# Performance work log

Hardware: AMD Instinct MI355X
Metric: run time of the kernel (lower is better)

The kernel has to match this reference:

```python
import jax, jax.numpy as jnp
import numpy as np

N_USERS = 50000
N_ITEMS = 50000
EMB_DIM = 64
N_EDGES = 1000000
N_LAYERS = 2
BATCH_SIZE = 50000
DECAY = 1e-4
NEG_SLOPE = 0.2


def setup_inputs() -> dict:
    key = jax.random.key(0)
    k1, k2, k3, k4, k5, k6 = jax.random.split(key, 6)
    return {
        "user_emb": jax.random.normal(k1, (N_USERS, EMB_DIM), dtype=jnp.float32) * 0.1,
        "item_emb": jax.random.normal(k2, (N_ITEMS, EMB_DIM), dtype=jnp.float32) * 0.1,
        "u_idx": jax.random.randint(k3, (N_EDGES,), 0, N_USERS),
        "i_idx": jax.random.randint(k4, (N_EDGES,), 0, N_ITEMS),
        "pos_items_ur": jax.random.randint(k5, (N_USERS,), 0, N_ITEMS),
        "neg_items_ur": jax.random.randint(k6, (N_USERS,), 0, N_ITEMS),
    }


def _segment_attn_sum(src_emb_g, e, dst, num_segments):
    # GAT-style: a = softmax_over_dst_mailbox(leaky_relu(e)); out = sum a * src_emb
    a = jax.nn.leaky_relu(e, NEG_SLOPE)
    m = jax.ops.segment_max(a, dst, num_segments=num_segments)
    m = jnp.where(jnp.isfinite(m), m, 0.0)  # empty segments -> -inf; never gathered but keep clean
    ex = jnp.exp(a - m[dst])
    den = jax.ops.segment_sum(ex, dst, num_segments=num_segments)
    w = ex / den[dst]  # den > 0 wherever an edge exists
    return jax.ops.segment_sum(w[:, None] * src_emb_g, dst, num_segments=num_segments)


def _gat_layer(user_emb, item_emb, u_idx, i_idx):
    # edge score e = <src_emb, dst_emb>, symmetric for both directions
    ue = user_emb[u_idx]           # [E, D]
    ie = item_emb[i_idx]           # [E, D]
    e = jnp.sum(ue * ie, axis=-1)  # [E]
    new_user = _segment_attn_sum(ie, e, u_idx, user_emb.shape[0])  # item -> user
    new_item = _segment_attn_sum(ue, e, i_idx, item_emb.shape[0])  # user -> item
    return new_user, new_item


def _inference(user_emb, item_emb, u_idx, i_idx):
    users = [user_emb]
    items = [item_emb]
    u, it = user_emb, item_emb
    for _ in range(N_LAYERS):
        u, it = _gat_layer(u, it, u_idx, i_idx)
        users.append(u)
        items.append(it)
    user_out = jnp.mean(jnp.stack(users, axis=1), axis=1)
    item_out = jnp.mean(jnp.stack(items, axis=1), axis=1)
    return user_out, item_out


def reference(user_emb, item_emb, u_idx, i_idx, pos_items_ur, neg_items_ur):
    user_out, item_out = _inference(user_emb, item_emb, u_idx, i_idx)
    users = user_out
    pos = item_out[pos_items_ur]
    neg = item_out[neg_items_ur]
    pos_scores = jnp.sum(users * pos, axis=1)
    neg_scores = jnp.sum(users * neg, axis=1)
    regularizer = 0.5 * (jnp.sum(users ** 2) + jnp.sum(pos ** 2) + jnp.sum(neg ** 2))
    regularizer = regularizer / BATCH_SIZE
    mf_loss = jnp.mean(jax.nn.softplus(neg_scores - pos_scores))
    emb_loss = DECAY * regularizer
    return jnp.stack([mf_loss, emb_loss])
```

## Files before the change

kernel.cpp:

```cpp
#include <hip/hip_runtime.h>
#include <math.h>

#define D 64
#define NEG_SLOPE 0.2f
#define DECAY_C 1e-4f
#define BKT_CAP 8192
#define K1_CHUNK 4096

__device__ __forceinline__ unsigned short f2bf(float f) {
  unsigned int u = __float_as_uint(f);
  u += 0x7FFFu + ((u >> 16) & 1u);
  return (unsigned short)(u >> 16);
}
__device__ __forceinline__ float bflo(unsigned int u) {
  return __uint_as_float(u << 16);
}
__device__ __forceinline__ float bfhi(unsigned int u) {
  return __uint_as_float(u & 0xFFFF0000u);
}

__global__ __launch_bounds__(256) void partition_kernel(
    const int* __restrict__ uidx, const int* __restrict__ iidx, int E,
    int nbktU, int nbktI, int* __restrict__ gCurU, int* __restrict__ gCurI,
    unsigned int* __restrict__ recU, unsigned int* __restrict__ recI,
    int npart, const float4* __restrict__ uemb,
    const float4* __restrict__ iemb, unsigned short* __restrict__ ubf,
    unsigned short* __restrict__ ibf, int nu4, int ni4) {
  if ((int)blockIdx.x >= npart) {
    int stride = ((int)gridDim.x - npart) * 256;
    int total = nu4 + ni4;
    for (int k = ((int)blockIdx.x - npart) * 256 + (int)threadIdx.x; k < total;
         k += stride) {
      bool isu = k < nu4;
      int idx = isu ? k : k - nu4;
      float4 v = isu ? uemb[idx] : iemb[idx];
      ushort4 o;
      o.x = f2bf(v.x);
      o.y = f2bf(v.y);
      o.z = f2bf(v.z);
      o.w = f2bf(v.w);
      *(ushort4*)((isu ? ubf : ibf) + (size_t)idx * 4) = o;
    }
    return;
  }
  __shared__ int uu[K1_CHUNK], ii[K1_CHUNK];
  __shared__ int histU[256], histI[256], baseU[256], baseI[256];
  int e0 = blockIdx.x * K1_CHUNK;
  int cnt = min(K1_CHUNK, E - e0);
  int t = threadIdx.x;
  for (int k = t; k < cnt; k += 256) {
    uu[k] = uidx[e0 + k];
    ii[k] = iidx[e0 + k];
  }
  histU[t] = 0;
  histI[t] = 0;
  __syncthreads();
  for (int k = t; k < cnt; k += 256) {
    atomicAdd(&histU[uu[k] >> 8], 1);
    atomicAdd(&histI[ii[k] >> 8], 1);
  }
  __syncthreads();
  {
    int h = histU[t];
    baseU[t] = (t < nbktU && h) ? atomicAdd(&gCurU[t], h) : 0;
    h = histI[t];
    baseI[t] = (t < nbktI && h) ? atomicAdd(&gCurI[t], h) : 0;
  }
  __syncthreads();
  histU[t] = 0;
  histI[t] = 0;
  __syncthreads();
  for (int k = t; k < cnt; k += 256) {
    int u = uu[k], it = ii[k];
    int b = u >> 8;
    int ofs = baseU[b] + atomicAdd(&histU[b], 1);
    if (ofs < BKT_CAP)
      recU[(size_t)b * BKT_CAP + ofs] =
          ((unsigned int)(u & 255) << 16) | (unsigned int)it;
    b = it >> 8;
    ofs = baseI[b] + atomicAdd(&histI[b], 1);
    if (ofs < BKT_CAP)
      recI[(size_t)b * BKT_CAP + ofs] =
          ((unsigned int)(it & 255) << 16) | (unsigned int)u;
  }
}

__global__ __launch_bounds__(256) void csr_kernel(
    const int* __restrict__ gCurU, const int* __restrict__ gCurI,
    const unsigned int* __restrict__ recU, const unsigned int* __restrict__ recI,
    unsigned short* __restrict__ srcU, unsigned short* __restrict__ srcI,
    int2* __restrict__ rowU, int2* __restrict__ rowI, int nbktU, int nbktI,
    int NUc, int NIc) {
  int bid = blockIdx.x;
  bool isU = bid < nbktU;
  int bkt = isU ? bid : bid - nbktU;
  const unsigned int* rec = (isU ? recU : recI) + (size_t)bkt * BKT_CAP;
  unsigned short* gsrc = (isU ? srcU : srcI) + (size_t)bkt * BKT_CAP;
  int2* rowspan = isU ? rowU : rowI;
  int N = isU ? NUc : NIc;
  int cnt = min((isU ? gCurU : gCurI)[bkt], BKT_CAP);

  __shared__ unsigned int lrec[BKT_CAP];
  __shared__ unsigned short sbuf[BKT_CAP];
  __shared__ int hist[256], excl[256], wsum[4];
  int t = threadIdx.x;
  hist[t] = 0;
  for (int k = t; k < cnt; k += 256) lrec[k] = rec[k];
  __syncthreads();
  for (int k = t; k < cnt; k += 256) atomicAdd(&hist[lrec[k] >> 16], 1);
  __syncthreads();
  int v = hist[t];
  int lane = t & 63, wid = t >> 6;
  int s = v;
#pragma unroll
  for (int off = 1; off < 64; off <<= 1) {
    int tv = __shfl_up(s, off);
    if (lane >= off) s += tv;
  }
  if (lane == 63) wsum[wid] = s;
  __syncthreads();
  if (t == 0) {
    int a = 0;
#pragma unroll
    for (int w = 0; w < 4; ++w) {
      int x = wsum[w];
      wsum[w] = a;
      a += x;
    }
  }
  __syncthreads();
  int ex = s - v + wsum[wid];
  excl[t] = ex;
  int n = bkt * 256 + t;
  if (n < N) rowspan[n] = make_int2(bkt * BKT_CAP + ex, v);
  __syncthreads();
  hist[t] = 0;
  __syncthreads();
  for (int k = t; k < cnt; k += 256) {
    unsigned int r = lrec[k];
    int loc = r >> 16;
    int ofs = atomicAdd(&hist[loc], 1);
    sbuf[excl[loc] + ofs] = (unsigned short)(r & 0xFFFFu);
  }
  __syncthreads();
  for (int k = t; k < cnt; k += 256) gsrc[k] = sbuf[k];
}

__global__ __launch_bounds__(256) void gat_walk_kernel(
    const unsigned short* __restrict__ dU, const unsigned short* __restrict__ dI,
    const int2* __restrict__ rowU, const unsigned short* __restrict__ srcU,
    const int2* __restrict__ rowI, const unsigned short* __restrict__ srcI,
    const float4* __restrict__ e0U, const float4* __restrict__ e0I,
    unsigned short* __restrict__ obU, unsigned short* __restrict__ obI,
    float4* __restrict__ omU, float4* __restrict__ omI, int NUc, int NIc) {
  int lane8 = threadIdx.x & 7;
  int gid = ((int)blockIdx.x * (int)blockDim.x + (int)threadIdx.x) >> 3;
  int ngroups = ((int)gridDim.x * (int)blockDim.x) >> 3;
  int Ntot = NUc + NIc;
  for (int node = gid; node < Ntot; node += ngroups) {
    bool ud = node < NUc;
    int n = ud ? node : node - NUc;
    const unsigned short* demb = ud ? dU : dI;
    const unsigned short* semb = ud ? dI : dU;
    int2 span = (ud ? rowU : rowI)[n];
    const unsigned short* gsrc = ud ? srcU : srcI;
    int beg = span.x, deg = span.y;

    uint4 dv = *(const uint4*)(demb + (size_t)n * D + lane8 * 8);
    float ds[8];
    ds[0] = bflo(dv.x); ds[1] = bfhi(dv.x);
    ds[2] = bflo(dv.y); ds[3] = bfhi(dv.y);
    ds[4] = bflo(dv.z); ds[5] = bfhi(dv.z);
    ds[6] = bflo(dv.w); ds[7] = bfhi(dv.w);

    float den = 0.f;
    float acc[8] = {0.f, 0.f, 0.f, 0.f, 0.f, 0.f, 0.f, 0.f};
    for (int tb = 0; tb < deg; tb += 8) {
      int nb = deg - tb;
      if (nb > 8) nb = 8;
      int sidv = (lane8 < nb) ? (int)gsrc[beg + tb + lane8] : 0;
#pragma unroll 4
      for (int j = 0; j < nb; ++j) {
        int sj = __shfl(sidv, j, 8);
        uint4 rv = *(const uint4*)(semb + (size_t)sj * D + lane8 * 8);
        float r[8];
        r[0] = bflo(rv.x); r[1] = bfhi(rv.x);
        r[2] = bflo(rv.y); r[3] = bfhi(rv.y);
        r[4] = bflo(rv.z); r[5] = bfhi(rv.z);
        r[6] = bflo(rv.w); r[7] = bfhi(rv.w);
        float d = ds[0] * r[0] + ds[1] * r[1] + ds[2] * r[2] + ds[3] * r[3] +
                  ds[4] * r[4] + ds[5] * r[5] + ds[6] * r[6] + ds[7] * r[7];
        d += __shfl_xor(d, 4, 8);
        d += __shfl_xor(d, 2, 8);
        d += __shfl_xor(d, 1, 8);
        float a = (d > 0.f) ? d : NEG_SLOPE * d;
        float w = __expf(a);
        den += w;
#pragma unroll
        for (int q = 0; q < 8; ++q) acc[q] = fmaf(w, r[q], acc[q]);
      }
    }
    float inv = (den > 0.f) ? 1.f / den : 0.f;
    if (e0U != nullptr) {
      const float4* e0 = ud ? e0U : e0I;
      float4* om = ud ? omU : omI;
      size_t o = (size_t)n * 16 + lane8 * 2;
      float4 z0 = e0[o], z1 = e0[o + 1];
      float4 o0, o1;
      o0.x = (z0.x + ds[0] + acc[0] * inv) * (1.f / 3.f);
      o0.y = (z0.y + ds[1] + acc[1] * inv) * (1.f / 3.f);
      o0.z = (z0.z + ds[2] + acc[2] * inv) * (1.f / 3.f);
      o0.w = (z0.w + ds[3] + acc[3] * inv) * (1.f / 3.f);
      o1.x = (z1.x + ds[4] + acc[4] * inv) * (1.f / 3.f);
      o1.y = (z1.y + ds[5] + acc[5] * inv) * (1.f / 3.f);
      o1.z = (z1.z + ds[6] + acc[6] * inv) * (1.f / 3.f);
      o1.w = (z1.w + ds[7] + acc[7] * inv) * (1.f / 3.f);
      om[o] = o0;
      om[o + 1] = o1;
    } else {
      unsigned short* ob = ud ? obU : obI;
      uint4 ov;
      ov.x = (unsigned int)f2bf(acc[0] * inv) |
             ((unsigned int)f2bf(acc[1] * inv) << 16);
      ov.y = (unsigned int)f2bf(acc[2] * inv) |
             ((unsigned int)f2bf(acc[3] * inv) << 16);
      ov.z = (unsigned int)f2bf(acc[4] * inv) |
             ((unsigned int)f2bf(acc[5] * inv) << 16);
      ov.w = (unsigned int)f2bf(acc[6] * inv) |
             ((unsigned int)f2bf(acc[7] * inv) << 16);
      *(uint4*)(ob + (size_t)n * D + lane8 * 8) = ov;
    }
  }
}

__global__ __launch_bounds__(256) void loss_kernel(
    const float4* __restrict__ um, const float4* __restrict__ im,
    const int* __restrict__ pos_idx, const int* __restrict__ neg_idx,
    float* __restrict__ acc, int N) {
  int lane16 = threadIdx.x & 15;
  int gid = ((int)blockIdx.x * (int)blockDim.x + (int)threadIdx.x) >> 4;
  int ngroups = ((int)gridDim.x * (int)blockDim.x) >> 4;
  float mf = 0.f, rg = 0.f;
  for (int n = gid; n < N; n += ngroups) {
    float4 us = um[(size_t)n * 16 + lane16];
    int p = pos_idx[n], q = neg_idx[n];
    float4 ps = im[(size_t)p * 16 + lane16];
    float4 ng = im[(size_t)q * 16 + lane16];
    float dps = us.x * ps.x + us.y * ps.y + us.z * ps.z + us.w * ps.w;
    float dns = us.x * ng.x + us.y * ng.y + us.z * ng.z + us.w * ng.w;
    float r = us.x * us.x + us.y * us.y + us.z * us.z + us.w * us.w +
              ps.x * ps.x + ps.y * ps.y + ps.z * ps.z + ps.w * ps.w +
              ng.x * ng.x + ng.y * ng.y + ng.z * ng.z + ng.w * ng.w;
#pragma unroll
    for (int off = 8; off >= 1; off >>= 1) {
      dps += __shfl_xor(dps, off, 16);
      dns += __shfl_xor(dns, off, 16);
      r += __shfl_xor(r, off, 16);
    }
    float x = dns - dps;
    float sp = fmaxf(x, 0.f) + log1pf(__expf(-fabsf(x)));
    mf += sp;
    rg += r;
  }
  __shared__ float smf[4], srg[4];
  int lane = threadIdx.x & 63;
  float wmf = (lane16 == 0) ? mf : 0.f;
  float wrg = (lane16 == 0) ? rg : 0.f;
  wmf += __shfl_xor(wmf, 16);
  wrg += __shfl_xor(wrg, 16);
  wmf += __shfl_xor(wmf, 32);
  wrg += __shfl_xor(wrg, 32);
  int wid = threadIdx.x >> 6;
  if (lane == 0) {
    smf[wid] = wmf;
    srg[wid] = wrg;
  }
  __syncthreads();
  if (threadIdx.x == 0) {
    atomicAdd(acc + 0, smf[0] + smf[1] + smf[2] + smf[3]);
    atomicAdd(acc + 1, srg[0] + srg[1] + srg[2] + srg[3]);
  }
}

__global__ void finalize_kernel(const float* __restrict__ acc,
                                float* __restrict__ out, float invN,
                                float regscale) {
  out[0] = acc[0] * invN;
  out[1] = acc[1] * regscale;
}

extern "C" void kernel_launch(void* const* d_in, const int* in_sizes, int n_in,
                              void* d_out, int out_size, void* d_ws,
                              size_t ws_size, hipStream_t stream) {
  const float* uemb = (const float*)d_in[0];
  const float* iemb = (const float*)d_in[1];
  const int* uidx = (const int*)d_in[2];
  const int* iidx = (const int*)d_in[3];
  const int* pos = (const int*)d_in[4];
  const int* neg = (const int*)d_in[5];
  const int NU = in_sizes[0] / D;
  const int NI = in_sizes[1] / D;
  const int E = in_sizes[2];
  const int NB = in_sizes[4];
  const int NBKT_U = (NU + 255) >> 8;
  const int NBKT_I = (NI + 255) >> 8;
  const int NPART = (E + K1_CHUNK - 1) / K1_CHUNK;

  char* ws = (char*)d_ws;
  size_t off = 0;
  auto alloc = [&](size_t bytes) -> void* {
    void* p = ws + off;
    off += (bytes + 255) & ~(size_t)255;
    return p;
  };
  int* gCur = (int*)alloc((size_t)(NBKT_U + NBKT_I) * 4);
  int* gCurU = gCur;
  int* gCurI = gCur + NBKT_U;
  unsigned int* recU = (unsigned int*)alloc((size_t)NBKT_U * BKT_CAP * 4);
  unsigned int* recI = (unsigned int*)alloc((size_t)NBKT_I * BKT_CAP * 4);
  unsigned short* srcU = (unsigned short*)recU;
  unsigned short* srcI = (unsigned short*)recI;
  int2* rowU = (int2*)alloc((size_t)NU * 8);
  int2* rowI = (int2*)alloc((size_t)NI * 8);
  unsigned short* ubf = (unsigned short*)alloc((size_t)NU * D * 2);
  unsigned short* ibf = (unsigned short*)alloc((size_t)NI * D * 2);
  unsigned short* u1 = (unsigned short*)alloc((size_t)NU * D * 2);
  unsigned short* i1 = (unsigned short*)alloc((size_t)NI * D * 2);
  float* um = (float*)alloc((size_t)NU * D * 4);
  float* im = (float*)alloc((size_t)NI * D * 4);
  float* acc = (float*)alloc(256);

  hipMemsetAsync(gCur, 0, (size_t)(NBKT_U + NBKT_I) * 4, stream);
  hipMemsetAsync(acc, 0, 8, stream);

  partition_kernel<<<NPART + 256, 256, 0, stream>>>(
      uidx, iidx, E, NBKT_U, NBKT_I, gCurU, gCurI, recU, recI, NPART,
      (const float4*)uemb, (const float4*)iemb, ubf, ibf, NU * 16, NI * 16);
  csr_kernel<<<NBKT_U + NBKT_I, 256, 0, stream>>>(
      gCurU, gCurI, recU, recI, srcU, srcI, rowU, rowI, NBKT_U, NBKT_I, NU,
      NI);

  gat_walk_kernel<<<4096, 256, 0, stream>>>(
      ubf, ibf, rowU, srcU, rowI, srcI, (const float4*)nullptr,
      (const float4*)nullptr, u1, i1, (float4*)nullptr, (float4*)nullptr, NU,
      NI);

  gat_walk_kernel<<<4096, 256, 0, stream>>>(
      u1, i1, rowU, srcU, rowI, srcI, (const float4*)uemb,
      (const float4*)iemb, (unsigned short*)nullptr, (unsigned short*)nullptr,
      (float4*)um, (float4*)im, NU, NI);

  loss_kernel<<<1024, 256, 0, stream>>>((const float4*)um, (const float4*)im,
                                        pos, neg, acc, NU);
  finalize_kernel<<<1, 1, 0, stream>>>(acc, (float*)d_out, 1.f / (float)NU,
                                       0.5f * DECAY_C / (float)NB);
}
```

Baseline: 171.9 us.

## Sort nodes by degree within buckets and batch neighbor gathers in GAT walk

The CSR kernel now counting-sorts the 256 nodes of each bucket by degree and writes an order array. The walk kernel iterates over that order, so the 8-lane groups in a wavefront handle nodes of similar degree and diverge less. The inner loop also issues all up-to-8 neighbor row loads before computing on them, raising memory-level parallelism at the cost of more registers. Padded slots are skipped through a sentinel value.

```diff
diff --git a/kernel.cpp b/kernel.cpp
--- a/kernel.cpp
+++ b/kernel.cpp
@@ -89,7 +89,8 @@
     const int* __restrict__ gCurU, const int* __restrict__ gCurI,
     const unsigned int* __restrict__ recU, const unsigned int* __restrict__ recI,
     unsigned short* __restrict__ srcU, unsigned short* __restrict__ srcI,
-    int2* __restrict__ rowU, int2* __restrict__ rowI, int nbktU, int nbktI,
+    int2* __restrict__ rowU, int2* __restrict__ rowI,
+    int* __restrict__ ordU, int* __restrict__ ordI, int nbktU, int nbktI,
     int NUc, int NIc) {
   int bid = blockIdx.x;
   bool isU = bid < nbktU;
@@ -97,6 +98,7 @@
   const unsigned int* rec = (isU ? recU : recI) + (size_t)bkt * BKT_CAP;
   unsigned short* gsrc = (isU ? srcU : srcI) + (size_t)bkt * BKT_CAP;
   int2* rowspan = isU ? rowU : rowI;
+  int* ord = (isU ? ordU : ordI) + bkt * 256;
   int N = isU ? NUc : NIc;
   int cnt = min((isU ? gCurU : gCurI)[bkt], BKT_CAP);
 
@@ -144,22 +146,54 @@
   }
   __syncthreads();
   for (int k = t; k < cnt; k += 256) gsrc[k] = sbuf[k];
+  __syncthreads();
+
+  hist[t] = 0;
+  __syncthreads();
+  int db = min(v, 255);
+  int slot = atomicAdd(&hist[db], 1);
+  __syncthreads();
+  int dv = hist[t];
+  int ds2 = dv;
+#pragma unroll
+  for (int off = 1; off < 64; off <<= 1) {
+    int tv = __shfl_up(ds2, off);
+    if (lane >= off) ds2 += tv;
+  }
+  if (lane == 63) wsum[wid] = ds2;
+  __syncthreads();
+  if (t == 0) {
+    int a = 0;
+#pragma unroll
+    for (int w = 0; w < 4; ++w) {
+      int x = wsum[w];
+      wsum[w] = a;
+      a += x;
+    }
+  }
+  __syncthreads();
+  excl[t] = ds2 - dv + wsum[wid];
+  __syncthreads();
+  ord[excl[db] + slot] = (n < N) ? n : 0x7FFFFFFF;
 }
 
 __global__ __launch_bounds__(256) void gat_walk_kernel(
     const unsigned short* __restrict__ dU, const unsigned short* __restrict__ dI,
     const int2* __restrict__ rowU, const unsigned short* __restrict__ srcU,
     const int2* __restrict__ rowI, const unsigned short* __restrict__ srcI,
+    const int* __restrict__ ordU, const int* __restrict__ ordI,
     const float4* __restrict__ e0U, const float4* __restrict__ e0I,
     unsigned short* __restrict__ obU, unsigned short* __restrict__ obI,
-    float4* __restrict__ omU, float4* __restrict__ omI, int NUc, int NIc) {
+    float4* __restrict__ omU, float4* __restrict__ omI, int slotU, int slotI,
+    int NUc, int NIc) {
   int lane8 = threadIdx.x & 7;
   int gid = ((int)blockIdx.x * (int)blockDim.x + (int)threadIdx.x) >> 3;
   int ngroups = ((int)gridDim.x * (int)blockDim.x) >> 3;
-  int Ntot = NUc + NIc;
-  for (int node = gid; node < Ntot; node += ngroups) {
-    bool ud = node < NUc;
-    int n = ud ? node : node - NUc;
+  int Stot = slotU + slotI;
+  for (int sidx = gid; sidx < Stot; sidx += ngroups) {
+    bool ud = sidx < slotU;
+    int n = ud ? ordU[sidx] : ordI[sidx - slotU];
+    if (n >= (ud ? NUc : NIc)) continue;
     const unsigned short* demb = ud ? dU : dI;
     const unsigned short* semb = ud ? dI : dU;
     int2 span = (ud ? rowU : rowI)[n];
@@ -179,25 +213,32 @@
       int nb = deg - tb;
       if (nb > 8) nb = 8;
       int sidv = (lane8 < nb) ? (int)gsrc[beg + tb + lane8] : 0;
-#pragma unroll 4
-      for (int j = 0; j < nb; ++j) {
-        int sj = __shfl(sidv, j, 8);
-        uint4 rv = *(const uint4*)(semb + (size_t)sj * D + lane8 * 8);
-        float r[8];
-        r[0] = bflo(rv.x); r[1] = bfhi(rv.x);
-        r[2] = bflo(rv.y); r[3] = bfhi(rv.y);
-        r[4] = bflo(rv.z); r[5] = bfhi(rv.z);
-        r[6] = bflo(rv.w); r[7] = bfhi(rv.w);
-        float d = ds[0] * r[0] + ds[1] * r[1] + ds[2] * r[2] + ds[3] * r[3] +
-                  ds[4] * r[4] + ds[5] * r[5] + ds[6] * r[6] + ds[7] * r[7];
-        d += __shfl_xor(d, 4, 8);
-        d += __shfl_xor(d, 2, 8);
-        d += __shfl_xor(d, 1, 8);
-        float a = (d > 0.f) ? d : NEG_SLOPE * d;
-        float w = __expf(a);
-        den += w;
-#pragma unroll
-        for (int q = 0; q < 8; ++q) acc[q] = fmaf(w, r[q], acc[q]);
+      int sj[8];
+#pragma unroll
+      for (int j = 0; j < 8; ++j) sj[j] = __shfl(sidv, j, 8);
+      uint4 rv[8];
+#pragma unroll
+      for (int j = 0; j < 8; ++j)
+        if (j < nb) rv[j] = *(const uint4*)(semb + (size_t)sj[j] * D + lane8 * 8);
+#pragma unroll
+      for (int j = 0; j < 8; ++j) {
+        if (j < nb) {
+          float r[8];
+          r[0] = bflo(rv[j].x); r[1] = bfhi(rv[j].x);
+          r[2] = bflo(rv[j].y); r[3] = bfhi(rv[j].y);
+          r[4] = bflo(rv[j].z); r[5] = bfhi(rv[j].z);
+          r[6] = bflo(rv[j].w); r[7] = bfhi(rv[j].w);
+          float d = ds[0] * r[0] + ds[1] * r[1] + ds[2] * r[2] + ds[3] * r[3] +
+                    ds[4] * r[4] + ds[5] * r[5] + ds[6] * r[6] + ds[7] * r[7];
+          d += __shfl_xor(d, 4, 8);
+          d += __shfl_xor(d, 2, 8);
+          d += __shfl_xor(d, 1, 8);
+          float a = fmaxf(d, NEG_SLOPE * d);
+          float w = __expf(a);
+          den += w;
+#pragma unroll
+          for (int q = 0; q < 8; ++q) acc[q] = fmaf(w, r[q], acc[q]);
+        }
       }
     }
     float inv = (den > 0.f) ? 1.f / den : 0.f;
@@ -322,6 +363,8 @@
   unsigned short* srcI = (unsigned short*)recI;
   int2* rowU = (int2*)alloc((size_t)NU * 8);
   int2* rowI = (int2*)alloc((size_t)NI * 8);
+  int* ordU = (int*)alloc((size_t)NBKT_U * 256 * 4);
+  int* ordI = (int*)alloc((size_t)NBKT_I * 256 * 4);
   unsigned short* ubf = (unsigned short*)alloc((size_t)NU * D * 2);
   unsigned short* ibf = (unsigned short*)alloc((size_t)NI * D * 2);
   unsigned short* u1 = (unsigned short*)alloc((size_t)NU * D * 2);
@@ -337,18 +380,20 @@
       uidx, iidx, E, NBKT_U, NBKT_I, gCurU, gCurI, recU, recI, NPART,
       (const float4*)uemb, (const float4*)iemb, ubf, ibf, NU * 16, NI * 16);
   csr_kernel<<<NBKT_U + NBKT_I, 256, 0, stream>>>(
-      gCurU, gCurI, recU, recI, srcU, srcI, rowU, rowI, NBKT_U, NBKT_I, NU,
-      NI);
+      gCurU, gCurI, recU, recI, srcU, srcI, rowU, rowI, ordU, ordI, NBKT_U,
+      NBKT_I, NU, NI);
+
+  const int SLOT_U = NBKT_U * 256, SLOT_I = NBKT_I * 256;
 
   gat_walk_kernel<<<4096, 256, 0, stream>>>(
-      ubf, ibf, rowU, srcU, rowI, srcI, (const float4*)nullptr,
-      (const float4*)nullptr, u1, i1, (float4*)nullptr, (float4*)nullptr, NU,
-      NI);
+      ubf, ibf, rowU, srcU, rowI, srcI, ordU, ordI, (const float4*)nullptr,
+      (const float4*)nullptr, u1, i1, (float4*)nullptr, (float4*)nullptr,
+      SLOT_U, SLOT_I, NU, NI);
 
   gat_walk_kernel<<<4096, 256, 0, stream>>>(
-      u1, i1, rowU, srcU, rowI, srcI, (const float4*)uemb,
+      u1, i1, rowU, srcU, rowI, srcI, ordU, ordI, (const float4*)uemb,
       (const float4*)iemb, (unsigned short*)nullptr, (unsigned short*)nullptr,
-      (float4*)um, (float4*)im, NU, NI);
+      (float4*)um, (float4*)im, SLOT_U, SLOT_I, NU, NI);
 
   loss_kernel<<<1024, 256, 0, stream>>>((const float4*)um, (const float4*)im,
                                         pos, neg, acc, NU);
```

Result: slower. 201.4 us (+17.2%).

## Batch neighbor gathers, add nontemporal loads/stores, one node per group in walk

Applied to the files above, without the earlier changes.

The neighbor loop in the GAT walk kernel now issues all up-to-8 gathered embedding loads before any compute, so more memory requests are in flight per lane group. Streaming loads and stores across the partition, CSR, walk and loss kernels become nontemporal hints, which keeps gathered embedding rows in cache. The walk grid is resized so each 8-lane group handles exactly one node instead of grid-striding. The batched gather adds register pressure (eight 16-byte vectors per lane), which may lower occupancy.

```diff
diff --git a/kernel.cpp b/kernel.cpp
--- a/kernel.cpp
+++ b/kernel.cpp
@@ -7,6 +7,11 @@
 #define BKT_CAP 8192
 #define K1_CHUNK 4096
 
+typedef unsigned int u32x4 __attribute__((ext_vector_type(4)));
+typedef unsigned short u16x4 __attribute__((ext_vector_type(4)));
+typedef float f32x4 __attribute__((ext_vector_type(4)));
+typedef int i32x2 __attribute__((ext_vector_type(2)));
+
 __device__ __forceinline__ unsigned short f2bf(float f) {
   unsigned int u = __float_as_uint(f);
   u += 0x7FFFu + ((u >> 16) & 1u);
@@ -23,9 +28,9 @@
     const int* __restrict__ uidx, const int* __restrict__ iidx, int E,
     int nbktU, int nbktI, int* __restrict__ gCurU, int* __restrict__ gCurI,
     unsigned int* __restrict__ recU, unsigned int* __restrict__ recI,
-    int npart, const float4* __restrict__ uemb,
-    const float4* __restrict__ iemb, unsigned short* __restrict__ ubf,
-    unsigned short* __restrict__ ibf, int nu4, int ni4) {
+    int npart, const float* __restrict__ uemb, const float* __restrict__ iemb,
+    unsigned short* __restrict__ ubf, unsigned short* __restrict__ ibf,
+    int nu4, int ni4) {
   if ((int)blockIdx.x >= npart) {
     int stride = ((int)gridDim.x - npart) * 256;
     int total = nu4 + ni4;
@@ -33,13 +38,15 @@
          k += stride) {
       bool isu = k < nu4;
       int idx = isu ? k : k - nu4;
-      float4 v = isu ? uemb[idx] : iemb[idx];
-      ushort4 o;
+      f32x4 v = __builtin_nontemporal_load(
+          (const f32x4*)(isu ? uemb : iemb) + idx);
+      u16x4 o;
       o.x = f2bf(v.x);
       o.y = f2bf(v.y);
       o.z = f2bf(v.z);
       o.w = f2bf(v.w);
-      *(ushort4*)((isu ? ubf : ibf) + (size_t)idx * 4) = o;
+      __builtin_nontemporal_store(
+          o, (u16x4*)((isu ? ubf : ibf) + (size_t)idx * 4));
     }
     return;
   }
@@ -49,8 +56,8 @@
   int cnt = min(K1_CHUNK, E - e0);
   int t = threadIdx.x;
   for (int k = t; k < cnt; k += 256) {
-    uu[k] = uidx[e0 + k];
-    ii[k] = iidx[e0 + k];
+    uu[k] = __builtin_nontemporal_load(&uidx[e0 + k]);
+    ii[k] = __builtin_nontemporal_load(&iidx[e0 + k]);
   }
   histU[t] = 0;
   histI[t] = 0;
@@ -89,14 +96,14 @@
     const int* __restrict__ gCurU, const int* __restrict__ gCurI,
     const unsigned int* __restrict__ recU, const unsigned int* __restrict__ recI,
     unsigned short* __restrict__ srcU, unsigned short* __restrict__ srcI,
-    int2* __restrict__ rowU, int2* __restrict__ rowI, int nbktU, int nbktI,
+    i32x2* __restrict__ rowU, i32x2* __restrict__ rowI, int nbktU, int nbktI,
     int NUc, int NIc) {
   int bid = blockIdx.x;
   bool isU = bid < nbktU;
   int bkt = isU ? bid : bid - nbktU;
   const unsigned int* rec = (isU ? recU : recI) + (size_t)bkt * BKT_CAP;
   unsigned short* gsrc = (isU ? srcU : srcI) + (size_t)bkt * BKT_CAP;
-  int2* rowspan = isU ? rowU : rowI;
+  i32x2* rowspan = isU ? rowU : rowI;
   int N = isU ? NUc : NIc;
   int cnt = min((isU ? gCurU : gCurI)[bkt], BKT_CAP);
 
@@ -105,7 +112,8 @@
   __shared__ int hist[256], excl[256], wsum[4];
   int t = threadIdx.x;
   hist[t] = 0;
-  for (int k = t; k < cnt; k += 256) lrec[k] = rec[k];
+  for (int k = t; k < cnt; k += 256)
+    lrec[k] = __builtin_nontemporal_load(&rec[k]);
   __syncthreads();
   for (int k = t; k < cnt; k += 256) atomicAdd(&hist[lrec[k] >> 16], 1);
   __syncthreads();
@@ -132,7 +140,12 @@
   int ex = s - v + wsum[wid];
   excl[t] = ex;
   int n = bkt * 256 + t;
-  if (n < N) rowspan[n] = make_int2(bkt * BKT_CAP + ex, v);
+  if (n < N) {
+    i32x2 sp;
+    sp.x = bkt * BKT_CAP + ex;
+    sp.y = v;
+    rowspan[n] = sp;
+  }
   __syncthreads();
   hist[t] = 0;
   __syncthreads();
@@ -143,16 +156,17 @@
     sbuf[excl[loc] + ofs] = (unsigned short)(r & 0xFFFFu);
   }
   __syncthreads();
-  for (int k = t; k < cnt; k += 256) gsrc[k] = sbuf[k];
+  for (int k = t; k < cnt; k += 256)
+    __builtin_nontemporal_store(sbuf[k], &gsrc[k]);
 }
 
 __global__ __launch_bounds__(256) void gat_walk_kernel(
     const unsigned short* __restrict__ dU, const unsigned short* __restrict__ dI,
-    const int2* __restrict__ rowU, const unsigned short* __restrict__ srcU,
-    const int2* __restrict__ rowI, const unsigned short* __restrict__ srcI,
-    const float4* __restrict__ e0U, const float4* __restrict__ e0I,
+    const i32x2* __restrict__ rowU, const unsigned short* __restrict__ srcU,
+    const i32x2* __restrict__ rowI, const unsigned short* __restrict__ srcI,
+    const float* __restrict__ e0U, const float* __restrict__ e0I,
     unsigned short* __restrict__ obU, unsigned short* __restrict__ obI,
-    float4* __restrict__ omU, float4* __restrict__ omI, int NUc, int NIc) {
+    float* __restrict__ omU, float* __restrict__ omI, int NUc, int NIc) {
   int lane8 = threadIdx.x & 7;
   int gid = ((int)blockIdx.x * (int)blockDim.x + (int)threadIdx.x) >> 3;
   int ngroups = ((int)gridDim.x * (int)blockDim.x) >> 3;
@@ -162,11 +176,12 @@
     int n = ud ? node : node - NUc;
     const unsigned short* demb = ud ? dU : dI;
     const unsigned short* semb = ud ? dI : dU;
-    int2 span = (ud ? rowU : rowI)[n];
+    i32x2 span = __builtin_nontemporal_load(&(ud ? rowU : rowI)[n]);
     const unsigned short* gsrc = ud ? srcU : srcI;
     int beg = span.x, deg = span.y;
 
-    uint4 dv = *(const uint4*)(demb + (size_t)n * D + lane8 * 8);
+    u32x4 dv = __builtin_nontemporal_load(
+        (const u32x4*)(demb + (size_t)n * D + lane8 * 8));
     float ds[8];
     ds[0] = bflo(dv.x); ds[1] = bfhi(dv.x);
     ds[2] = bflo(dv.y); ds[3] = bfhi(dv.y);
@@ -178,35 +193,46 @@
     for (int tb = 0; tb < deg; tb += 8) {
       int nb = deg - tb;
       if (nb > 8) nb = 8;
-      int sidv = (lane8 < nb) ? (int)gsrc[beg + tb + lane8] : 0;
-#pragma unroll 4
-      for (int j = 0; j < nb; ++j) {
-        int sj = __shfl(sidv, j, 8);
-        uint4 rv = *(const uint4*)(semb + (size_t)sj * D + lane8 * 8);
-        float r[8];
-        r[0] = bflo(rv.x); r[1] = bfhi(rv.x);
-        r[2] = bflo(rv.y); r[3] = bfhi(rv.y);
-        r[4] = bflo(rv.z); r[5] = bfhi(rv.z);
-        r[6] = bflo(rv.w); r[7] = bfhi(rv.w);
-        float d = ds[0] * r[0] + ds[1] * r[1] + ds[2] * r[2] + ds[3] * r[3] +
-                  ds[4] * r[4] + ds[5] * r[5] + ds[6] * r[6] + ds[7] * r[7];
-        d += __shfl_xor(d, 4, 8);
-        d += __shfl_xor(d, 2, 8);
-        d += __shfl_xor(d, 1, 8);
-        float a = (d > 0.f) ? d : NEG_SLOPE * d;
-        float w = __expf(a);
-        den += w;
-#pragma unroll
-        for (int q = 0; q < 8; ++q) acc[q] = fmaf(w, r[q], acc[q]);
+      int sidv = (lane8 < nb)
+                     ? (int)__builtin_nontemporal_load(&gsrc[beg + tb + lane8])
+                     : 0;
+      int sj[8];
+#pragma unroll
+      for (int j = 0; j < 8; ++j) sj[j] = __shfl(sidv, j, 8);
+      u32x4 rv[8];
+#pragma unroll
+      for (int j = 0; j < 8; ++j)
+        if (j < nb)
+          rv[j] = *(const u32x4*)(semb + (size_t)sj[j] * D + lane8 * 8);
+#pragma unroll
+      for (int j = 0; j < 8; ++j) {
+        if (j < nb) {
+          float r[8];
+          r[0] = bflo(rv[j].x); r[1] = bfhi(rv[j].x);
+          r[2] = bflo(rv[j].y); r[3] = bfhi(rv[j].y);
+          r[4] = bflo(rv[j].z); r[5] = bfhi(rv[j].z);
+          r[6] = bflo(rv[j].w); r[7] = bfhi(rv[j].w);
+          float d = ds[0] * r[0] + ds[1] * r[1] + ds[2] * r[2] + ds[3] * r[3] +
+                    ds[4] * r[4] + ds[5] * r[5] + ds[6] * r[6] + ds[7] * r[7];
+          d += __shfl_xor(d, 4, 8);
+          d += __shfl_xor(d, 2, 8);
+          d += __shfl_xor(d, 1, 8);
+          float a = fmaxf(d, NEG_SLOPE * d);
+          float w = __expf(a);
+          den += w;
+#pragma unroll
+          for (int q = 0; q < 8; ++q) acc[q] = fmaf(w, r[q], acc[q]);
+        }
       }
     }
     float inv = (den > 0.f) ? 1.f / den : 0.f;
     if (e0U != nullptr) {
-      const float4* e0 = ud ? e0U : e0I;
-      float4* om = ud ? omU : omI;
+      const f32x4* e0 = (const f32x4*)(ud ? e0U : e0I);
+      f32x4* om = (f32x4*)(ud ? omU : omI);
       size_t o = (size_t)n * 16 + lane8 * 2;
-      float4 z0 = e0[o], z1 = e0[o + 1];
-      float4 o0, o1;
+      f32x4 z0 = __builtin_nontemporal_load(&e0[o]);
+      f32x4 z1 = __builtin_nontemporal_load(&e0[o + 1]);
+      f32x4 o0, o1;
       o0.x = (z0.x + ds[0] + acc[0] * inv) * (1.f / 3.f);
       o0.y = (z0.y + ds[1] + acc[1] * inv) * (1.f / 3.f);
       o0.z = (z0.z + ds[2] + acc[2] * inv) * (1.f / 3.f);
@@ -215,11 +241,11 @@
       o1.y = (z1.y + ds[5] + acc[5] * inv) * (1.f / 3.f);
       o1.z = (z1.z + ds[6] + acc[6] * inv) * (1.f / 3.f);
       o1.w = (z1.w + ds[7] + acc[7] * inv) * (1.f / 3.f);
-      om[o] = o0;
-      om[o + 1] = o1;
+      __builtin_nontemporal_store(o0, &om[o]);
+      __builtin_nontemporal_store(o1, &om[o + 1]);
     } else {
       unsigned short* ob = ud ? obU : obI;
-      uint4 ov;
+      u32x4 ov;
       ov.x = (unsigned int)f2bf(acc[0] * inv) |
              ((unsigned int)f2bf(acc[1] * inv) << 16);
       ov.y = (unsigned int)f2bf(acc[2] * inv) |
@@ -228,24 +254,27 @@
              ((unsigned int)f2bf(acc[5] * inv) << 16);
       ov.w = (unsigned int)f2bf(acc[6] * inv) |
              ((unsigned int)f2bf(acc[7] * inv) << 16);
-      *(uint4*)(ob + (size_t)n * D + lane8 * 8) = ov;
+      __builtin_nontemporal_store(
+          ov, (u32x4*)(ob + (size_t)n * D + lane8 * 8));
     }
   }
 }
 
 __global__ __launch_bounds__(256) void loss_kernel(
-    const float4* __restrict__ um, const float4* __restrict__ im,
+    const float* __restrict__ umf, const float* __restrict__ imf,
     const int* __restrict__ pos_idx, const int* __restrict__ neg_idx,
     float* __restrict__ acc, int N) {
+  const f32x4* um = (const f32x4*)umf;
+  const f32x4* im = (const f32x4*)imf;
   int lane16 = threadIdx.x & 15;
   int gid = ((int)blockIdx.x * (int)blockDim.x + (int)threadIdx.x) >> 4;
   int ngroups = ((int)gridDim.x * (int)blockDim.x) >> 4;
   float mf = 0.f, rg = 0.f;
   for (int n = gid; n < N; n += ngroups) {
-    float4 us = um[(size_t)n * 16 + lane16];
+    f32x4 us = __builtin_nontemporal_load(&um[(size_t)n * 16 + lane16]);
     int p = pos_idx[n], q = neg_idx[n];
-    float4 ps = im[(size_t)p * 16 + lane16];
-    float4 ng = im[(size_t)q * 16 + lane16];
+    f32x4 ps = im[(size_t)p * 16 + lane16];
+    f32x4 ng = im[(size_t)q * 16 + lane16];
     float dps = us.x * ps.x + us.y * ps.y + us.z * ps.z + us.w * ps.w;
     float dns = us.x * ng.x + us.y * ng.y + us.z * ng.z + us.w * ng.w;
     float r = us.x * us.x + us.y * us.y + us.z * us.z + us.w * us.w +
@@ -320,8 +349,8 @@
   unsigned int* recI = (unsigned int*)alloc((size_t)NBKT_I * BKT_CAP * 4);
   unsigned short* srcU = (unsigned short*)recU;
   unsigned short* srcI = (unsigned short*)recI;
-  int2* rowU = (int2*)alloc((size_t)NU * 8);
-  int2* rowI = (int2*)alloc((size_t)NI * 8);
+  i32x2* rowU = (i32x2*)alloc((size_t)NU * 8);
+  i32x2* rowI = (i32x2*)alloc((size_t)NI * 8);
   unsigned short* ubf = (unsigned short*)alloc((size_t)NU * D * 2);
   unsigned short* ibf = (unsigned short*)alloc((size_t)NI * D * 2);
   unsigned short* u1 = (unsigned short*)alloc((size_t)NU * D * 2);
@@ -334,24 +363,23 @@
   hipMemsetAsync(acc, 0, 8, stream);
 
   partition_kernel<<<NPART + 256, 256, 0, stream>>>(
-      uidx, iidx, E, NBKT_U, NBKT_I, gCurU, gCurI, recU, recI, NPART,
-      (const float4*)uemb, (const float4*)iemb, ubf, ibf, NU * 16, NI * 16);
+      uidx, iidx, E, NBKT_U, NBKT_I, gCurU, gCurI, recU, recI, NPART, uemb,
+      iemb, ubf, ibf, NU * 16, NI * 16);
   csr_kernel<<<NBKT_U + NBKT_I, 256, 0, stream>>>(
       gCurU, gCurI, recU, recI, srcU, srcI, rowU, rowI, NBKT_U, NBKT_I, NU,
       NI);
 
-  gat_walk_kernel<<<4096, 256, 0, stream>>>(
-      ubf, ibf, rowU, srcU, rowI, srcI, (const float4*)nullptr,
-      (const float4*)nullptr, u1, i1, (float4*)nullptr, (float4*)nullptr, NU,
-      NI);
-
-  gat_walk_kernel<<<4096, 256, 0, stream>>>(
-      u1, i1, rowU, srcU, rowI, srcI, (const float4*)uemb,
-      (const float4*)iemb, (unsigned short*)nullptr, (unsigned short*)nullptr,
-      (float4*)um, (float4*)im, NU, NI);
-
-  loss_kernel<<<1024, 256, 0, stream>>>((const float4*)um, (const float4*)im,
-                                        pos, neg, acc, NU);
+  const int WBLK = (NU + NI + 31) / 32;
+
+  gat_walk_kernel<<<WBLK, 256, 0, stream>>>(
+      ubf, ibf, rowU, srcU, rowI, srcI, (const float*)nullptr,
+      (const float*)nullptr, u1, i1, (float*)nullptr, (float*)nullptr, NU, NI);
+
+  gat_walk_kernel<<<WBLK, 256, 0, stream>>>(
+      u1, i1, rowU, srcU, rowI, srcI, uemb, iemb, (unsigned short*)nullptr,
+      (unsigned short*)nullptr, um, im, NU, NI);
+
+  loss_kernel<<<1024, 256, 0, stream>>>(um, im, pos, neg, acc, NU);
   finalize_kernel<<<1, 1, 0, stream>>>(acc, (float*)d_out, 1.f / (float)NU,
                                        0.5f * DECAY_C / (float)NB);
 }
```

Result: slower. 234.8 us (+36.6%).
